# Kernel tuning notes

Hardware: AMD Instinct MI355X
Metric: run time of the kernel (lower is better)

Reference implementation:

```python
import jax, jax.numpy as jnp
import numpy as np

REG = 1.0
LAM1 = REG * 0.1
LAM2 = REG * 0.15
TAU = 0.01
RHO = 1.99
SIGMA = 1.0 / TAU / 72.0


def epsilon(I):
    # I: (c,h,w,2) -> G: (c,h,w,4); symmetrized gradient stencil
    I0, I1 = I[..., 0], I[..., 1]
    g0 = I0 - jnp.pad(I0[:, :-1, :], ((0, 0), (1, 0), (0, 0)))
    g1 = jnp.pad(I0[:, :, 1:] - I0[:, :, :-1], ((0, 0), (0, 0), (1, 0)))
    g2 = I1 - jnp.pad(I1[:, :, :-1], ((0, 0), (0, 0), (1, 0)))
    g3 = jnp.pad(I1[:, 1:, :] - I1[:, :-1, :], ((0, 0), (0, 1), (0, 0)))
    return jnp.stack([g0, g1, g2, g3], axis=-1)


def epsilonT(G):
    # G: (c,h,w,4) -> I: (c,h,w,2); adjoint of epsilon
    g0, g1, g2, g3 = G[..., 0], G[..., 1], G[..., 2], G[..., 3]
    i0 = g0 - jnp.pad(g0[:, 1:, :], ((0, 0), (0, 1), (0, 0)))
    A = g1[:, :, 1:]
    i0 = i0 + jnp.pad(A, ((0, 0), (0, 0), (1, 0))) - jnp.pad(A, ((0, 0), (0, 0), (0, 1)))
    i1 = g2 - jnp.pad(g2[:, :, 1:], ((0, 0), (0, 0), (0, 1)))
    B = g3[:, :-1, :]
    i1 = i1 + jnp.pad(B, ((0, 0), (1, 0), (0, 0))) - jnp.pad(B, ((0, 0), (0, 1), (0, 0)))
    return jnp.stack([i0, i1], axis=-1)


def nabla(I):
    # I: (c,h,w) -> G: (c,h,w,2); forward differences, zero at far boundary
    g0 = jnp.pad(I[:, 1:, :] - I[:, :-1, :], ((0, 0), (0, 1), (0, 0)))
    g1 = jnp.pad(I[:, :, 1:] - I[:, :, :-1], ((0, 0), (0, 0), (0, 1)))
    return jnp.stack([g0, g1], axis=-1)


def nablaT(G):
    # G: (c,h,w,2) -> I: (c,h,w); negative divergence (adjoint of nabla)
    A = G[:, :-1, :, 0]
    B = G[:, :, :-1, 1]
    return (jnp.pad(A, ((0, 0), (1, 0), (0, 0))) - jnp.pad(A, ((0, 0), (0, 1), (0, 0)))
            + jnp.pad(B, ((0, 0), (0, 0), (1, 0))) - jnp.pad(B, ((0, 0), (0, 0), (0, 1))))


def prox_tau_fx(x, y):
    return (x + TAU * y) / (1.0 + TAU)


def prox_tau_fr(r):
    left = jnp.sqrt(jnp.sum(r ** 2, axis=3)) / (TAU * LAM1)
    return r - r / jnp.maximum(left, 1.0)[..., None]


def prox_sigma_g_conj(u):
    return u / jnp.maximum(jnp.sqrt(jnp.sum(u ** 2, axis=3)) / LAM2, 1.0)[..., None]


def setup_inputs() -> dict:
    key = jax.random.key(0)
    y = jax.random.normal(key, (3, 512, 512), dtype=jnp.float32)
    return {"y": y, "n_it_max": 30}


def reference(y, n_it_max):
    c, h, w = y.shape
    x2 = y
    r2 = jnp.zeros((c, h, w, 2), dtype=y.dtype)
    u2 = jnp.zeros((c, h, w, 4), dtype=y.dtype)

    def step(carry, _):
        x2, r2, u2 = carry
        tmp = TAU * epsilonT(u2)
        x = prox_tau_fx(x2 - nablaT(tmp), y)
        r = prox_tau_fr(r2 + tmp)
        u = prox_sigma_g_conj(u2 + SIGMA * epsilon(nabla(2.0 * x - x2) - (2.0 * r - r2)))
        x2 = x2 + RHO * (x - x2)
        r2 = r2 + RHO * (r - r2)
        u2 = u2 + RHO * (u - u2)
        return (x2, r2, u2), None

    (x2, r2, u2), _ = jax.lax.scan(step, (x2, r2, u2), None, length=n_it_max)
    return (x2, r2, u2)
```

## Files before the change

kernel.cpp:

```cpp
#include <hip/hip_runtime.h>
#include <type_traits>


#define H 512
#define W 512
#define C 3
#define HW (H * W)
#define CHW (C * H * W)
#define N_IT 30

#define TW 64
#define TH 16

#define TAU     0.01f
#define LAM2    0.15f
#define RHO     1.99f
#define SIGMA   1.3888888888888888f
#define TL1     0.001f
#define INV_1PT (1.0f / 1.01f)

#define BROWS 18
#define BSTR  72

typedef _Float16 f16;
typedef __attribute__((ext_vector_type(4))) _Float16 h4;
typedef __attribute__((ext_vector_type(8))) _Float16 h8;


template <int MODE>
__global__ __launch_bounds__(384)
void fused_it(const float* __restrict__ y,
              const float* __restrict__ srcX,
              const f16*   __restrict__ srcH,
              float*       __restrict__ dstX,
              f16*         __restrict__ dstH,
              float*       __restrict__ outp)
{
    __shared__ float sb[3][BROWS][BSTR];

    const int tid = threadIdx.x;
    const int c   = blockIdx.z;
    const int i0  = blockIdx.y * TH;
    const int j0  = blockIdx.x * TW;
    const int cb  = c * HW;

    const bool edge = (MODE == 0) ||
                      (blockIdx.x == 0) || (blockIdx.x == W / TW - 1) ||
                      (blockIdx.y == 0) || (blockIdx.y == H / TH - 1);

    const f16* rSrc = srcH;
    const f16* uSrc = srcH + 2 * CHW;
    f16* rDst = dstH;
    f16* uDst = dstH ? dstH + 2 * CHW : nullptr;

    float cu0[4], cu1[4], cu2[4], cu3[4];
    float xbO[4], rb0O[4], rb1O[4];

    auto strip1 = [&](auto SAFE_c, int rr, int s, bool interior) {
        constexpr bool SAFE = decltype(SAFE_c)::value;
        const int gi  = i0 + rr;
        const int gjb = j0 + s;
        const int p   = cb + gi * W + gjb;

        const bool rowC  = SAFE || ((unsigned)gi < H);
        const bool cMain = SAFE || ((unsigned)gjb < W);
        const bool okC   = rowC && cMain;

        float yv[4], x2c[4], r0c[4], r1c[4];
        if (okC) {
            *(float4*)yv = *(const float4*)(y + p);
        } else {
            yv[0] = yv[1] = yv[2] = yv[3] = 0.f;
        }
        if (MODE != 0) {
            if (okC) {
                *(float4*)x2c = *(const float4*)(srcX + p);
                const h8 rv = *(const h8*)(rSrc + 2 * p);
                #pragma unroll
                for (int e = 0; e < 4; ++e) {
                    r0c[e] = (float)rv[2 * e];
                    r1c[e] = (float)rv[2 * e + 1];
                }
            } else {
                #pragma unroll
                for (int e = 0; e < 4; ++e) { x2c[e] = 0.f; r0c[e] = 0.f; r1c[e] = 0.f; }
            }
        }

        float t0c[4], t1c[4], t0n[4], t1w[4];
        if (MODE == 0) {
            #pragma unroll
            for (int e = 0; e < 4; ++e) {
                x2c[e] = yv[e]; r0c[e] = 0.f; r1c[e] = 0.f;
                t0c[e] = t1c[e] = t0n[e] = t1w[e] = 0.f;
            }
            if (interior) {
                #pragma unroll
                for (int e = 0; e < 4; ++e) { cu0[e] = cu1[e] = cu2[e] = cu3[e] = 0.f; }
            }
        } else {
            const bool rowN = SAFE || ((unsigned)(gi - 1) < H);
            const bool rowS = SAFE || ((unsigned)(gi + 1) < H);
            const bool cm1  = SAFE || ((unsigned)(gjb - 1) < W);
            const bool c4   = SAFE || ((unsigned)(gjb + 4) < W);
            const int pN = p - W, pS = p + W;

            auto L4 = [&](int pp, bool ok) -> h4 {
                h4 z = {}; if (ok) z = *(const h4*)(uSrc + 4 * pp); return z;
            };
            auto L8 = [&](int pp, bool ok) -> h8 {
                h8 z = {}; if (ok) z = *(const h8*)(uSrc + 4 * pp); return z;
            };
            const h4 nA = L4(pN - 1, rowN && cm1);
            const h8 nB = L8(pN,     rowN && cMain);
            const h8 nC = L8(pN + 2, rowN && cMain);
            const h4 nD = L4(pN + 4, rowN && c4);
            const h4 cA = L4(p - 1,  rowC && cm1);
            const h8 cB = L8(p,      okC);
            const h8 cC = L8(p + 2,  okC);
            const h4 cD = L4(p + 4,  rowC && c4);
            const h8 sB = L8(pS,     rowS && cMain);
            const h8 sC = L8(pS + 2, rowS && cMain);

            const float u0c[4] = {(float)cB[0], (float)cB[4], (float)cC[0], (float)cC[4]};
            const float u1c[5] = {(float)cB[1], (float)cB[5], (float)cC[1], (float)cC[5], (float)cD[1]};
            const float u2r[6] = {(float)cA[2], (float)cB[2], (float)cB[6], (float)cC[2], (float)cC[6], (float)cD[2]};
            const float u3c[5] = {(float)cA[3], (float)cB[3], (float)cB[7], (float)cC[3], (float)cC[7]};
            const float u0n[4] = {(float)nB[0], (float)nB[4], (float)nC[0], (float)nC[4]};
            const float u1n[5] = {(float)nB[1], (float)nB[5], (float)nC[1], (float)nC[5], (float)nD[1]};
            const float u3n[5] = {(float)nA[3], (float)nB[3], (float)nB[7], (float)nC[3], (float)nC[7]};
            const float u0s[4] = {(float)sB[0], (float)sB[4], (float)sC[0], (float)sC[4]};

            if constexpr (SAFE) {
                #pragma unroll
                for (int e = 0; e < 4; ++e) {
                    t0c[e] = TAU * (u0c[e] - u0s[e] + u1c[e] - u1c[e + 1]);
                    t1c[e] = TAU * (u2r[e + 1] - u2r[e + 2] + u3n[e + 1] - u3c[e + 1]);
                    t0n[e] = TAU * (u0n[e] - u0c[e] + u1n[e] - u1n[e + 1]);
                    t1w[e] = TAU * (u2r[e] - u2r[e + 1] + u3n[e] - u3c[e]);
                }
            } else {
                const bool im0 = gi > 0, imHl = gi < H - 1;
                #pragma unroll
                for (int e = 0; e < 4; ++e) {
                    const int gj = gjb + e;
                    const bool jm0 = gj > 0;
                    t0c[e] = TAU * (u0c[e] - u0s[e] + (jm0 ? u1c[e] : 0.f) - u1c[e + 1]);
                    t1c[e] = TAU * (u2r[e + 1] - u2r[e + 2] + u3n[e + 1] - (imHl ? u3c[e + 1] : 0.f));
                    t0n[e] = im0 ? TAU * (u0n[e] - u0c[e] + (jm0 ? u1n[e] : 0.f) - u1n[e + 1]) : 0.f;
                    t1w[e] = jm0 ? TAU * (u2r[e] - u2r[e + 1] + u3n[e] - (imHl ? u3c[e] : 0.f)) : 0.f;
                }
            }
            if (interior) {
                #pragma unroll
                for (int e = 0; e < 4; ++e) {
                    cu0[e] = u0c[e]; cu1[e] = u1c[e];
                    cu2[e] = u2r[e + 1]; cu3[e] = u3c[e + 1];
                }
            }
        }

        float xnew[4], rn0[4], rn1[4], xb[4], rb0[4], rb1[4];
        {
            const bool imH = SAFE ? true : (gi < H - 1);
            #pragma unroll
            for (int e = 0; e < 4; ++e) {
                const int gj = gjb + e;
                const bool jmW = SAFE ? true : (gj < W - 1);
                const float nT  = t0n[e] - (imH ? t0c[e] : 0.f) + t1w[e] - (jmW ? t1c[e] : 0.f);
                const float xv  = (x2c[e] - nT + TAU * yv[e]) * INV_1PT;
                xb[e] = 2.f * xv - x2c[e];
                const float rp0 = r0c[e] + t0c[e];
                const float rp1 = r1c[e] + t1c[e];
                const float ss  = rp0 * rp0 + rp1 * rp1;
                const float f   = 1.f - fminf(TL1 * rsqrtf(ss), 1.f);
                const float rv0 = rp0 * f, rv1 = rp1 * f;
                rb0[e]  = 2.f * rv0 - r0c[e];
                rb1[e]  = 2.f * rv1 - r1c[e];
                xnew[e] = x2c[e] + RHO * (xv - x2c[e]);
                rn0[e]  = r0c[e] + RHO * (rv0 - r0c[e]);
                rn1[e]  = r1c[e] + RHO * (rv1 - r1c[e]);
            }
        }
        *(float4*)&sb[0][rr + 1][s + 4] = *(float4*)xb;
        *(float4*)&sb[1][rr + 1][s + 4] = *(float4*)rb0;
        *(float4*)&sb[2][rr + 1][s + 4] = *(float4*)rb1;

        if (interior) {
            #pragma unroll
            for (int e = 0; e < 4; ++e) {
                xbO[e] = xb[e]; rb0O[e] = rb0[e]; rb1O[e] = rb1[e];
            }
            if (MODE == 2) {
                *(float4*)(outp + p) = *(float4*)xnew;
                *(float4*)(outp + CHW + 2 * p)     = make_float4(rn0[0], rn1[0], rn0[1], rn1[1]);
                *(float4*)(outp + CHW + 2 * p + 4) = make_float4(rn0[2], rn1[2], rn0[3], rn1[3]);
            } else {
                *(float4*)(dstX + p) = *(float4*)xnew;
                h8 hr;
                #pragma unroll
                for (int e = 0; e < 4; ++e) {
                    hr[2 * e]     = (f16)rn0[e];
                    hr[2 * e + 1] = (f16)rn1[e];
                }
                *(h8*)(rDst + 2 * p) = hr;
            }
        }
    };

    auto ringmap = [&](int t, int& rr, int& s) {
        if (t < 18)      { rr = -1;      s = 4 * t - 4; }
        else if (t < 36) { rr = TH;      s = 4 * (t - 18) - 4; }
        else if (t < 36 + TH) { rr = t - 36;      s = -4; }
        else                  { rr = t - 36 - TH; s = TW; }
    };

    if (!edge) {
        if (tid < 256) {
            strip1(std::true_type{}, tid >> 4, 4 * (tid & 15), true);
        } else if (tid < 256 + 36 + 2 * TH) {
            int rr, s; ringmap(tid - 256, rr, s);
            strip1(std::true_type{}, rr, s, false);
        }
    } else {
        if (tid < 256) {
            strip1(std::false_type{}, tid >> 4, 4 * (tid & 15), true);
        } else if (tid < 256 + 36 + 2 * TH) {
            int rr, s; ringmap(tid - 256, rr, s);
            strip1(std::false_type{}, rr, s, false);
        }
    }
    __syncthreads();

    auto stage2 = [&](auto SAFE_c) {
        constexpr bool SAFE = decltype(SAFE_c)::value;
        const int tx = tid & 15, ty = tid >> 4;
        const int gi  = i0 + ty;
        const int gjb = j0 + 4 * tx;
        const int lr  = ty + 1;
        const int lc  = 4 * tx + 4;
        float4 v;
        float xA[6], xS[6], xN[4], r0C[5], r0N[4], r1C[5], r1S[4];
        xA[0] = sb[0][lr][lc - 1];
        xA[1] = xbO[0]; xA[2] = xbO[1]; xA[3] = xbO[2]; xA[4] = xbO[3];
        xA[5] = sb[0][lr][lc + 4];
        xS[0] = sb[0][lr + 1][lc - 1];
        v = *(const float4*)&sb[0][lr + 1][lc]; xS[1]=v.x; xS[2]=v.y; xS[3]=v.z; xS[4]=v.w;
        xS[5] = sb[0][lr + 1][lc + 4];
        v = *(const float4*)&sb[0][lr - 1][lc]; xN[0]=v.x; xN[1]=v.y; xN[2]=v.z; xN[3]=v.w;
        r0C[0] = sb[1][lr][lc - 1];
        r0C[1] = rb0O[0]; r0C[2] = rb0O[1]; r0C[3] = rb0O[2]; r0C[4] = rb0O[3];
        v = *(const float4*)&sb[1][lr - 1][lc]; r0N[0]=v.x; r0N[1]=v.y; r0N[2]=v.z; r0N[3]=v.w;
        r1C[0] = sb[2][lr][lc - 1];
        r1C[1] = rb1O[0]; r1C[2] = rb1O[1]; r1C[3] = rb1O[2]; r1C[4] = rb1O[3];
        v = *(const float4*)&sb[2][lr + 1][lc]; r1S[0]=v.x; r1S[1]=v.y; r1S[2]=v.z; r1S[3]=v.w;

        const bool im0 = SAFE ? true : (gi > 0);
        const bool imH = SAFE ? true : (gi < H - 1);
        float un0[4], un1[4], un2[4], un3[4];
        #pragma unroll
        for (int e = 0; e < 4; ++e) {
            const int gj = gjb + e;
            const bool jm0 = SAFE ? true : (gj > 0);
            const bool jmW = SAFE ? true : (gj < W - 1);
            const float xC = xA[e + 1], xE = xA[e + 2], xW_ = xA[e];
            const float I0c = (imH ? xS[e + 1] - xC : 0.f) - r0C[e + 1];
            const float I0n = im0 ? (xC - xN[e] - r0N[e]) : 0.f;
            const float I0w = jm0 ? ((imH ? xS[e] - xW_ : 0.f) - r0C[e]) : 0.f;
            const float I1c = (jmW ? xE - xC : 0.f) - r1C[e + 1];
            const float I1w = jm0 ? (xC - xW_ - r1C[e]) : 0.f;
            const float I1s = imH ? ((jmW ? xS[e + 2] - xS[e + 1] : 0.f) - r1S[e]) : 0.f;
            const float g0 = I0c - I0n;
            const float g1 = jm0 ? (I0c - I0w) : 0.f;
            const float g2 = I1c - I1w;
            const float g3 = imH ? (I1s - I1c) : 0.f;
            const float up0 = cu0[e] + SIGMA * g0;
            const float up1 = cu1[e] + SIGMA * g1;
            const float up2 = cu2[e] + SIGMA * g2;
            const float up3 = cu3[e] + SIGMA * g3;
            const float ss  = up0 * up0 + up1 * up1 + up2 * up2 + up3 * up3;
            const float inv = fminf(LAM2 * rsqrtf(ss), 1.f);
            un0[e] = cu0[e] + RHO * (up0 * inv - cu0[e]);
            un1[e] = cu1[e] + RHO * (up1 * inv - cu1[e]);
            un2[e] = cu2[e] + RHO * (up2 * inv - cu2[e]);
            un3[e] = cu3[e] + RHO * (up3 * inv - cu3[e]);
        }
        const int p = cb + gi * W + gjb;
        if (MODE == 2) {
            #pragma unroll
            for (int e = 0; e < 4; ++e)
                *(float4*)(outp + 3 * CHW + 4 * (p + e)) =
                    make_float4(un0[e], un1[e], un2[e], un3[e]);
        } else {
            h8 w0, w1;
            #pragma unroll
            for (int e = 0; e < 2; ++e) {
                w0[4 * e + 0] = (f16)un0[e]; w0[4 * e + 1] = (f16)un1[e];
                w0[4 * e + 2] = (f16)un2[e]; w0[4 * e + 3] = (f16)un3[e];
            }
            #pragma unroll
            for (int e = 2; e < 4; ++e) {
                w1[4 * (e - 2) + 0] = (f16)un0[e]; w1[4 * (e - 2) + 1] = (f16)un1[e];
                w1[4 * (e - 2) + 2] = (f16)un2[e]; w1[4 * (e - 2) + 3] = (f16)un3[e];
            }
            *(h8*)(uDst + 4 * p)     = w0;
            *(h8*)(uDst + 4 * p + 8) = w1;
        }
    };

    if (tid < 256) {
        if (!edge) stage2(std::true_type{});
        else       stage2(std::false_type{});
    }
}

extern "C" void kernel_launch(void* const* d_in, const int* in_sizes, int n_in,
                              void* d_out, int out_size, void* d_ws, size_t ws_size,
                              hipStream_t stream) {
    const float* y = (const float*)d_in[0];
    float* out = (float*)d_out;

    float* x0 = (float*)d_ws;
    float* x1 = x0 + CHW;
    f16*   h0 = (f16*)(x1 + CHW);
    f16*   h1 = h0 + 6 * CHW;

    dim3 blk(384, 1, 1);
    dim3 grd(W / TW, H / TH, C);

    fused_it<0><<<grd, blk, 0, stream>>>(y, nullptr, nullptr, x0, h0, nullptr);
    for (int k = 2; k < N_IT; ++k) {
        const bool even = (k % 2 == 0);
        float* sx = even ? x0 : x1;  f16* sh = even ? h0 : h1;
        float* dx = even ? x1 : x0;  f16* dh = even ? h1 : h0;
        fused_it<1><<<grd, blk, 0, stream>>>(y, sx, sh, dx, dh, nullptr);
    }
    fused_it<2><<<grd, blk, 0, stream>>>(y, x0, h0, nullptr, nullptr, out);
}
```

Measured before the change: 331.5 us.

## Fuse two PDHG iterations per kernel launch using halo tiles in shared memory

Result: faster. 299.7 us (median of 2 runs) (-9.6%).

```diff
diff --git a/kernel.cpp b/kernel.cpp
--- a/kernel.cpp
+++ b/kernel.cpp
@@ -7,7 +7,7 @@
 #define C 3
 #define HW (H * W)
 #define CHW (C * H * W)
-#define N_IT 30
+#define NPAIR 15
 
 #define TW 64
 #define TH 16
@@ -19,8 +19,12 @@
 #define TL1     0.001f
 #define INV_1PT (1.0f / 1.01f)
 
-#define BROWS 18
-#define BSTR  72
+#define AR 22
+#define AC 78
+#define BR 18
+#define BC 72
+#define UR 20
+#define UC 75
 
 typedef _Float16 f16;
 typedef __attribute__((ext_vector_type(4))) _Float16 h4;
@@ -28,15 +32,17 @@
 
 
 template <int MODE>
-__global__ __launch_bounds__(384)
-void fused_it(const float* __restrict__ y,
-              const float* __restrict__ srcX,
-              const f16*   __restrict__ srcH,
-              float*       __restrict__ dstX,
-              f16*         __restrict__ dstH,
-              float*       __restrict__ outp)
+__global__ __launch_bounds__(256)
+void fused2(const float* __restrict__ y,
+            const float* __restrict__ srcX,
+            const f16*   __restrict__ srcH,
+            float*       __restrict__ dstX,
+            f16*         __restrict__ dstH,
+            float*       __restrict__ outp)
 {
-    __shared__ float sb[3][BROWS][BSTR];
+    __shared__ float sbA[3][AR][AC];
+    __shared__ float sbB[3][BR][BC];
+    __shared__ f16   su[UR][UC][4];
 
     const int tid = threadIdx.x;
     const int c   = blockIdx.z;
@@ -53,211 +59,116 @@
     f16* rDst = dstH;
     f16* uDst = dstH ? dstH + 2 * CHW : nullptr;
 
-    float cu0[4], cu1[4], cu2[4], cu3[4];
-    float xbO[4], rb0O[4], rb1O[4];
-
-    auto strip1 = [&](auto SAFE_c, int rr, int s, bool interior) {
-        constexpr bool SAFE = decltype(SAFE_c)::value;
-        const int gi  = i0 + rr;
-        const int gjb = j0 + s;
-        const int p   = cb + gi * W + gjb;
-
+    auto prox1 = [&](auto SAFE_c, int gi, int gjb,
+                     const float* yv, const float* x2c, const float* r0c, const float* r1c,
+                     const float* t0c, const float* t1c, const float* t0n, const float* t1w,
+                     float* xb, float* rb0, float* rb1,
+                     float* xn, float* rn0, float* rn1) {
+        constexpr bool SAFE = decltype(SAFE_c)::value;
+        const bool imH = SAFE ? true : (gi < H - 1);
+        #pragma unroll
+        for (int e = 0; e < 4; ++e) {
+            const int gj = gjb + e;
+            const bool jmW = SAFE ? true : (gj < W - 1);
+            const float nT  = t0n[e] - (imH ? t0c[e] : 0.f) + t1w[e] - (jmW ? t1c[e] : 0.f);
+            const float xv  = (x2c[e] - nT + TAU * yv[e]) * INV_1PT;
+            xb[e] = 2.f * xv - x2c[e];
+            const float rp0 = r0c[e] + t0c[e];
+            const float rp1 = r1c[e] + t1c[e];
+            const float ss  = rp0 * rp0 + rp1 * rp1;
+            const float f   = 1.f - fminf(TL1 * rsqrtf(ss), 1.f);
+            const float rv0 = rp0 * f, rv1 = rp1 * f;
+            rb0[e] = 2.f * rv0 - r0c[e];
+            rb1[e] = 2.f * rv1 - r1c[e];
+            xn[e]  = x2c[e] + RHO * (xv - x2c[e]);
+            rn0[e] = r0c[e] + RHO * (rv0 - r0c[e]);
+            rn1[e] = r1c[e] + RHO * (rv1 - r1c[e]);
+        }
+    };
+
+    auto tGlob = [&](auto SAFE_c, int gi, int gjb, int p,
+                     float* t0c, float* t1c, float* t0n, float* t1w) {
+        constexpr bool SAFE = decltype(SAFE_c)::value;
         const bool rowC  = SAFE || ((unsigned)gi < H);
         const bool cMain = SAFE || ((unsigned)gjb < W);
         const bool okC   = rowC && cMain;
-
-        float yv[4], x2c[4], r0c[4], r1c[4];
-        if (okC) {
-            *(float4*)yv = *(const float4*)(y + p);
+        const bool rowN = SAFE || ((unsigned)(gi - 1) < H);
+        const bool rowS = SAFE || ((unsigned)(gi + 1) < H);
+        const bool cm1  = SAFE || ((unsigned)(gjb - 1) < W);
+        const bool c4   = SAFE || ((unsigned)(gjb + 4) < W);
+        const int pN = p - W, pS = p + W;
+        auto L4 = [&](int pp, bool ok) -> h4 { h4 z = {}; if (ok) z = *(const h4*)(uSrc + 4 * pp); return z; };
+        auto L8 = [&](int pp, bool ok) -> h8 { h8 z = {}; if (ok) z = *(const h8*)(uSrc + 4 * pp); return z; };
+        const h4 nA = L4(pN - 1, rowN && cm1);
+        const h8 nB = L8(pN,     rowN && cMain);
+        const h8 nC = L8(pN + 2, rowN && cMain);
+        const h4 nD = L4(pN + 4, rowN && c4);
+        const h4 cA = L4(p - 1,  rowC && cm1);
+        const h8 cB = L8(p,      okC);
+        const h8 cC = L8(p + 2,  okC);
+        const h4 cD = L4(p + 4,  rowC && c4);
+        const h8 sB = L8(pS,     rowS && cMain);
+        const h8 sC = L8(pS + 2, rowS && cMain);
+
+        const float u0c[4] = {(float)cB[0], (float)cB[4], (float)cC[0], (float)cC[4]};
+        const float u1c[5] = {(float)cB[1], (float)cB[5], (float)cC[1], (float)cC[5], (float)cD[1]};
+        const float u2r[6] = {(float)cA[2], (float)cB[2], (float)cB[6], (float)cC[2], (float)cC[6], (float)cD[2]};
+        const float u3c[5] = {(float)cA[3], (float)cB[3], (float)cB[7], (float)cC[3], (float)cC[7]};
+        const float u0n[4] = {(float)nB[0], (float)nB[4], (float)nC[0], (float)nC[4]};
+        const float u1n[5] = {(float)nB[1], (float)nB[5], (float)nC[1], (float)nC[5], (float)nD[1]};
+        const float u3n[5] = {(float)nA[3], (float)nB[3], (float)nB[7], (float)nC[3], (float)nC[7]};
+        const float u0s[4] = {(float)sB[0], (float)sB[4], (float)sC[0], (float)sC[4]};
+
+        if constexpr (SAFE) {
+            #pragma unroll
+            for (int e = 0; e < 4; ++e) {
+                t0c[e] = TAU * (u0c[e] - u0s[e] + u1c[e] - u1c[e + 1]);
+                t1c[e] = TAU * (u2r[e + 1] - u2r[e + 2] + u3n[e + 1] - u3c[e + 1]);
+                t0n[e] = TAU * (u0n[e] - u0c[e] + u1n[e] - u1n[e + 1]);
+                t1w[e] = TAU * (u2r[e] - u2r[e + 1] + u3n[e] - u3c[e]);
+            }
         } else {
-            yv[0] = yv[1] = yv[2] = yv[3] = 0.f;
-        }
-        if (MODE != 0) {
-            if (okC) {
-                *(float4*)x2c = *(const float4*)(srcX + p);
-                const h8 rv = *(const h8*)(rSrc + 2 * p);
-                #pragma unroll
-                for (int e = 0; e < 4; ++e) {
-                    r0c[e] = (float)rv[2 * e];
-                    r1c[e] = (float)rv[2 * e + 1];
-                }
-            } else {
-                #pragma unroll
-                for (int e = 0; e < 4; ++e) { x2c[e] = 0.f; r0c[e] = 0.f; r1c[e] = 0.f; }
-            }
-        }
-
-        float t0c[4], t1c[4], t0n[4], t1w[4];
-        if (MODE == 0) {
-            #pragma unroll
-            for (int e = 0; e < 4; ++e) {
-                x2c[e] = yv[e]; r0c[e] = 0.f; r1c[e] = 0.f;
-                t0c[e] = t1c[e] = t0n[e] = t1w[e] = 0.f;
-            }
-            if (interior) {
-                #pragma unroll
-                for (int e = 0; e < 4; ++e) { cu0[e] = cu1[e] = cu2[e] = cu3[e] = 0.f; }
-            }
-        } else {
-            const bool rowN = SAFE || ((unsigned)(gi - 1) < H);
-            const bool rowS = SAFE || ((unsigned)(gi + 1) < H);
-            const bool cm1  = SAFE || ((unsigned)(gjb - 1) < W);
-            const bool c4   = SAFE || ((unsigned)(gjb + 4) < W);
-            const int pN = p - W, pS = p + W;
-
-            auto L4 = [&](int pp, bool ok) -> h4 {
-                h4 z = {}; if (ok) z = *(const h4*)(uSrc + 4 * pp); return z;
-            };
-            auto L8 = [&](int pp, bool ok) -> h8 {
-                h8 z = {}; if (ok) z = *(const h8*)(uSrc + 4 * pp); return z;
-            };
-            const h4 nA = L4(pN - 1, rowN && cm1);
-            const h8 nB = L8(pN,     rowN && cMain);
-            const h8 nC = L8(pN + 2, rowN && cMain);
-            const h4 nD = L4(pN + 4, rowN && c4);
-            const h4 cA = L4(p - 1,  rowC && cm1);
-            const h8 cB = L8(p,      okC);
-            const h8 cC = L8(p + 2,  okC);
-            const h4 cD = L4(p + 4,  rowC && c4);
-            const h8 sB = L8(pS,     rowS && cMain);
-            const h8 sC = L8(pS + 2, rowS && cMain);
-
-            const float u0c[4] = {(float)cB[0], (float)cB[4], (float)cC[0], (float)cC[4]};
-            const float u1c[5] = {(float)cB[1], (float)cB[5], (float)cC[1], (float)cC[5], (float)cD[1]};
-            const float u2r[6] = {(float)cA[2], (float)cB[2], (float)cB[6], (float)cC[2], (float)cC[6], (float)cD[2]};
-            const float u3c[5] = {(float)cA[3], (float)cB[3], (float)cB[7], (float)cC[3], (float)cC[7]};
-            const float u0n[4] = {(float)nB[0], (float)nB[4], (float)nC[0], (float)nC[4]};
-            const float u1n[5] = {(float)nB[1], (float)nB[5], (float)nC[1], (float)nC[5], (float)nD[1]};
-            const float u3n[5] = {(float)nA[3], (float)nB[3], (float)nB[7], (float)nC[3], (float)nC[7]};
-            const float u0s[4] = {(float)sB[0], (float)sB[4], (float)sC[0], (float)sC[4]};
-
-            if constexpr (SAFE) {
-                #pragma unroll
-                for (int e = 0; e < 4; ++e) {
-                    t0c[e] = TAU * (u0c[e] - u0s[e] + u1c[e] - u1c[e + 1]);
-                    t1c[e] = TAU * (u2r[e + 1] - u2r[e + 2] + u3n[e + 1] - u3c[e + 1]);
-                    t0n[e] = TAU * (u0n[e] - u0c[e] + u1n[e] - u1n[e + 1]);
-                    t1w[e] = TAU * (u2r[e] - u2r[e + 1] + u3n[e] - u3c[e]);
-                }
-            } else {
-                const bool im0 = gi > 0, imHl = gi < H - 1;
-                #pragma unroll
-                for (int e = 0; e < 4; ++e) {
-                    const int gj = gjb + e;
-                    const bool jm0 = gj > 0;
-                    t0c[e] = TAU * (u0c[e] - u0s[e] + (jm0 ? u1c[e] : 0.f) - u1c[e + 1]);
-                    t1c[e] = TAU * (u2r[e + 1] - u2r[e + 2] + u3n[e + 1] - (imHl ? u3c[e + 1] : 0.f));
-                    t0n[e] = im0 ? TAU * (u0n[e] - u0c[e] + (jm0 ? u1n[e] : 0.f) - u1n[e + 1]) : 0.f;
-                    t1w[e] = jm0 ? TAU * (u2r[e] - u2r[e + 1] + u3n[e] - (imHl ? u3c[e] : 0.f)) : 0.f;
-                }
-            }
-            if (interior) {
-                #pragma unroll
-                for (int e = 0; e < 4; ++e) {
-                    cu0[e] = u0c[e]; cu1[e] = u1c[e];
-                    cu2[e] = u2r[e + 1]; cu3[e] = u3c[e + 1];
-                }
-            }
-        }
-
-        float xnew[4], rn0[4], rn1[4], xb[4], rb0[4], rb1[4];
-        {
-            const bool imH = SAFE ? true : (gi < H - 1);
+            const bool im0 = gi > 0, imHl = gi < H - 1;
             #pragma unroll
             for (int e = 0; e < 4; ++e) {
                 const int gj = gjb + e;
-                const bool jmW = SAFE ? true : (gj < W - 1);
-                const float nT  = t0n[e] - (imH ? t0c[e] : 0.f) + t1w[e] - (jmW ? t1c[e] : 0.f);
-                const float xv  = (x2c[e] - nT + TAU * yv[e]) * INV_1PT;
-                xb[e] = 2.f * xv - x2c[e];
-                const float rp0 = r0c[e] + t0c[e];
-                const float rp1 = r1c[e] + t1c[e];
-                const float ss  = rp0 * rp0 + rp1 * rp1;
-                const float f   = 1.f - fminf(TL1 * rsqrtf(ss), 1.f);
-                const float rv0 = rp0 * f, rv1 = rp1 * f;
-                rb0[e]  = 2.f * rv0 - r0c[e];
-                rb1[e]  = 2.f * rv1 - r1c[e];
-                xnew[e] = x2c[e] + RHO * (xv - x2c[e]);
-                rn0[e]  = r0c[e] + RHO * (rv0 - r0c[e]);
-                rn1[e]  = r1c[e] + RHO * (rv1 - r1c[e]);
-            }
-        }
-        *(float4*)&sb[0][rr + 1][s + 4] = *(float4*)xb;
-        *(float4*)&sb[1][rr + 1][s + 4] = *(float4*)rb0;
-        *(float4*)&sb[2][rr + 1][s + 4] = *(float4*)rb1;
-
-        if (interior) {
-            #pragma unroll
-            for (int e = 0; e < 4; ++e) {
-                xbO[e] = xb[e]; rb0O[e] = rb0[e]; rb1O[e] = rb1[e];
-            }
-            if (MODE == 2) {
-                *(float4*)(outp + p) = *(float4*)xnew;
-                *(float4*)(outp + CHW + 2 * p)     = make_float4(rn0[0], rn1[0], rn0[1], rn1[1]);
-                *(float4*)(outp + CHW + 2 * p + 4) = make_float4(rn0[2], rn1[2], rn0[3], rn1[3]);
-            } else {
-                *(float4*)(dstX + p) = *(float4*)xnew;
-                h8 hr;
-                #pragma unroll
-                for (int e = 0; e < 4; ++e) {
-                    hr[2 * e]     = (f16)rn0[e];
-                    hr[2 * e + 1] = (f16)rn1[e];
-                }
-                *(h8*)(rDst + 2 * p) = hr;
-            }
-        }
-    };
-
-    auto ringmap = [&](int t, int& rr, int& s) {
-        if (t < 18)      { rr = -1;      s = 4 * t - 4; }
-        else if (t < 36) { rr = TH;      s = 4 * (t - 18) - 4; }
-        else if (t < 36 + TH) { rr = t - 36;      s = -4; }
-        else                  { rr = t - 36 - TH; s = TW; }
-    };
-
-    if (!edge) {
-        if (tid < 256) {
-            strip1(std::true_type{}, tid >> 4, 4 * (tid & 15), true);
-        } else if (tid < 256 + 36 + 2 * TH) {
-            int rr, s; ringmap(tid - 256, rr, s);
-            strip1(std::true_type{}, rr, s, false);
-        }
-    } else {
-        if (tid < 256) {
-            strip1(std::false_type{}, tid >> 4, 4 * (tid & 15), true);
-        } else if (tid < 256 + 36 + 2 * TH) {
-            int rr, s; ringmap(tid - 256, rr, s);
-            strip1(std::false_type{}, rr, s, false);
-        }
-    }
-    __syncthreads();
-
-    auto stage2 = [&](auto SAFE_c) {
-        constexpr bool SAFE = decltype(SAFE_c)::value;
-        const int tx = tid & 15, ty = tid >> 4;
-        const int gi  = i0 + ty;
-        const int gjb = j0 + 4 * tx;
-        const int lr  = ty + 1;
-        const int lc  = 4 * tx + 4;
+                const bool jm0 = gj > 0;
+                t0c[e] = TAU * (u0c[e] - u0s[e] + (jm0 ? u1c[e] : 0.f) - u1c[e + 1]);
+                t1c[e] = TAU * (u2r[e + 1] - u2r[e + 2] + u3n[e + 1] - (imHl ? u3c[e + 1] : 0.f));
+                t0n[e] = im0 ? TAU * (u0n[e] - u0c[e] + (jm0 ? u1n[e] : 0.f) - u1n[e + 1]) : 0.f;
+                t1w[e] = jm0 ? TAU * (u2r[e] - u2r[e + 1] + u3n[e] - (imHl ? u3c[e] : 0.f)) : 0.f;
+            }
+        }
+    };
+
+    auto loadA = [&](int rr, int s,
+                     float* xA, float* xS, float* xN,
+                     float* r0C, float* r0N, float* r1C, float* r1S) {
+        const int lr = rr + 3, lc = s + 8;
         float4 v;
-        float xA[6], xS[6], xN[4], r0C[5], r0N[4], r1C[5], r1S[4];
-        xA[0] = sb[0][lr][lc - 1];
-        xA[1] = xbO[0]; xA[2] = xbO[1]; xA[3] = xbO[2]; xA[4] = xbO[3];
-        xA[5] = sb[0][lr][lc + 4];
-        xS[0] = sb[0][lr + 1][lc - 1];
-        v = *(const float4*)&sb[0][lr + 1][lc]; xS[1]=v.x; xS[2]=v.y; xS[3]=v.z; xS[4]=v.w;
-        xS[5] = sb[0][lr + 1][lc + 4];
-        v = *(const float4*)&sb[0][lr - 1][lc]; xN[0]=v.x; xN[1]=v.y; xN[2]=v.z; xN[3]=v.w;
-        r0C[0] = sb[1][lr][lc - 1];
-        r0C[1] = rb0O[0]; r0C[2] = rb0O[1]; r0C[3] = rb0O[2]; r0C[4] = rb0O[3];
-        v = *(const float4*)&sb[1][lr - 1][lc]; r0N[0]=v.x; r0N[1]=v.y; r0N[2]=v.z; r0N[3]=v.w;
-        r1C[0] = sb[2][lr][lc - 1];
-        r1C[1] = rb1O[0]; r1C[2] = rb1O[1]; r1C[3] = rb1O[2]; r1C[4] = rb1O[3];
-        v = *(const float4*)&sb[2][lr + 1][lc]; r1S[0]=v.x; r1S[1]=v.y; r1S[2]=v.z; r1S[3]=v.w;
-
+        xA[0] = sbA[0][lr][lc - 1];
+        v = *(const float4*)&sbA[0][lr][lc]; xA[1]=v.x; xA[2]=v.y; xA[3]=v.z; xA[4]=v.w;
+        xA[5] = sbA[0][lr][lc + 4];
+        xS[0] = sbA[0][lr + 1][lc - 1];
+        v = *(const float4*)&sbA[0][lr + 1][lc]; xS[1]=v.x; xS[2]=v.y; xS[3]=v.z; xS[4]=v.w;
+        xS[5] = sbA[0][lr + 1][lc + 4];
+        v = *(const float4*)&sbA[0][lr - 1][lc]; xN[0]=v.x; xN[1]=v.y; xN[2]=v.z; xN[3]=v.w;
+        r0C[0] = sbA[1][lr][lc - 1];
+        v = *(const float4*)&sbA[1][lr][lc]; r0C[1]=v.x; r0C[2]=v.y; r0C[3]=v.z; r0C[4]=v.w;
+        v = *(const float4*)&sbA[1][lr - 1][lc]; r0N[0]=v.x; r0N[1]=v.y; r0N[2]=v.z; r0N[3]=v.w;
+        r1C[0] = sbA[2][lr][lc - 1];
+        v = *(const float4*)&sbA[2][lr][lc]; r1C[1]=v.x; r1C[2]=v.y; r1C[3]=v.z; r1C[4]=v.w;
+        v = *(const float4*)&sbA[2][lr + 1][lc]; r1S[0]=v.x; r1S[1]=v.y; r1S[2]=v.z; r1S[3]=v.w;
+    };
+
+    auto s2core = [&](auto SAFE_c, int gi, int gjb,
+                      const float* xA, const float* xS, const float* xN,
+                      const float* r0C, const float* r0N, const float* r1C, const float* r1S,
+                      const float* cu0, const float* cu1, const float* cu2, const float* cu3,
+                      float* un0, float* un1, float* un2, float* un3) {
+        constexpr bool SAFE = decltype(SAFE_c)::value;
         const bool im0 = SAFE ? true : (gi > 0);
         const bool imH = SAFE ? true : (gi < H - 1);
-        float un0[4], un1[4], un2[4], un3[4];
         #pragma unroll
         for (int e = 0; e < 4; ++e) {
             const int gj = gjb + e;
@@ -285,7 +196,243 @@
             un2[e] = cu2[e] + RHO * (up2 * inv - cu2[e]);
             un3[e] = cu3[e] + RHO * (up3 * inv - cu3[e]);
         }
-        const int p = cb + gi * W + gjb;
+    };
+
+    auto phaseA = [&](auto SAFE_c) {
+        constexpr bool SAFE = decltype(SAFE_c)::value;
+        for (int idx = tid; idx < AR * 18; idx += 256) {
+            const int rw = idx / 18, rr = rw - 3;
+            const int s  = 4 * (idx - rw * 18) - 4;
+            const int gi = i0 + rr, gjb = j0 + s;
+            const int p  = cb + gi * W + gjb;
+            const bool rowC  = SAFE || ((unsigned)gi < H);
+            const bool cMain = SAFE || ((unsigned)gjb < W);
+            const bool okC   = rowC && cMain;
+
+            float yv[4], x2c[4], r0c[4], r1c[4];
+            if (okC) { *(float4*)yv = *(const float4*)(y + p); }
+            else     { yv[0] = yv[1] = yv[2] = yv[3] = 0.f; }
+
+            float t0c[4], t1c[4], t0n[4], t1w[4];
+            if (MODE == 0) {
+                #pragma unroll
+                for (int e = 0; e < 4; ++e) {
+                    x2c[e] = yv[e]; r0c[e] = 0.f; r1c[e] = 0.f;
+                    t0c[e] = t1c[e] = t0n[e] = t1w[e] = 0.f;
+                }
+            } else {
+                if (okC) {
+                    *(float4*)x2c = *(const float4*)(srcX + p);
+                    const h8 rv = *(const h8*)(rSrc + 2 * p);
+                    #pragma unroll
+                    for (int e = 0; e < 4; ++e) {
+                        r0c[e] = (float)rv[2 * e];
+                        r1c[e] = (float)rv[2 * e + 1];
+                    }
+                } else {
+                    #pragma unroll
+                    for (int e = 0; e < 4; ++e) { x2c[e] = 0.f; r0c[e] = 0.f; r1c[e] = 0.f; }
+                }
+                tGlob(SAFE_c, gi, gjb, p, t0c, t1c, t0n, t1w);
+            }
+
+            float xb[4], rb0[4], rb1[4], xn[4], rn0[4], rn1[4];
+            prox1(SAFE_c, gi, gjb, yv, x2c, r0c, r1c, t0c, t1c, t0n, t1w,
+                  xb, rb0, rb1, xn, rn0, rn1);
+
+            *(float4*)&sbA[0][rr + 3][s + 8] = *(float4*)xb;
+            *(float4*)&sbA[1][rr + 3][s + 8] = *(float4*)rb0;
+            *(float4*)&sbA[2][rr + 3][s + 8] = *(float4*)rb1;
+            if (rr >= -1 && rr <= 16) {
+                *(float4*)&sbB[0][rr + 1][s + 4] = *(float4*)xn;
+                *(float4*)&sbB[1][rr + 1][s + 4] = *(float4*)rn0;
+                *(float4*)&sbB[2][rr + 1][s + 4] = *(float4*)rn1;
+            }
+        }
+    };
+
+    auto phaseB = [&](auto SAFE_c) {
+        constexpr bool SAFE = decltype(SAFE_c)::value;
+        for (int idx = tid; idx < UR * 18; idx += 256) {
+            const int rw = idx / 18, rr = rw - 2;
+            const int s  = 4 * (idx - rw * 18) - 4;
+            const int gi = i0 + rr, gjb = j0 + s;
+            const int p  = cb + gi * W + gjb;
+
+            float xA[6], xS[6], xN[4], r0C[5], r0N[4], r1C[5], r1S[4];
+            loadA(rr, s, xA, xS, xN, r0C, r0N, r1C, r1S);
+
+            float cu0[4], cu1[4], cu2[4], cu3[4];
+            if (MODE == 0) {
+                #pragma unroll
+                for (int e = 0; e < 4; ++e) { cu0[e] = cu1[e] = cu2[e] = cu3[e] = 0.f; }
+            } else {
+                const bool okC = SAFE || (((unsigned)gi < H) && ((unsigned)gjb < W));
+                if (okC) {
+                    const h8 a = *(const h8*)(uSrc + 4 * p);
+                    const h8 b = *(const h8*)(uSrc + 4 * p + 8);
+                    cu0[0]=(float)a[0]; cu1[0]=(float)a[1]; cu2[0]=(float)a[2]; cu3[0]=(float)a[3];
+                    cu0[1]=(float)a[4]; cu1[1]=(float)a[5]; cu2[1]=(float)a[6]; cu3[1]=(float)a[7];
+                    cu0[2]=(float)b[0]; cu1[2]=(float)b[1]; cu2[2]=(float)b[2]; cu3[2]=(float)b[3];
+                    cu0[3]=(float)b[4]; cu1[3]=(float)b[5]; cu2[3]=(float)b[6]; cu3[3]=(float)b[7];
+                } else {
+                    #pragma unroll
+                    for (int e = 0; e < 4; ++e) { cu0[e] = cu1[e] = cu2[e] = cu3[e] = 0.f; }
+                }
+            }
+
+            float un0[4], un1[4], un2[4], un3[4];
+            s2core(SAFE_c, gi, gjb, xA, xS, xN, r0C, r0N, r1C, r1S,
+                   cu0, cu1, cu2, cu3, un0, un1, un2, un3);
+
+            const int ur = rr + 2, uc = s + 6;
+            if constexpr (SAFE) {
+                h8 w0, w1;
+                #pragma unroll
+                for (int e = 0; e < 2; ++e) {
+                    w0[4*e+0]=(f16)un0[e]; w0[4*e+1]=(f16)un1[e];
+                    w0[4*e+2]=(f16)un2[e]; w0[4*e+3]=(f16)un3[e];
+                }
+                #pragma unroll
+                for (int e = 2; e < 4; ++e) {
+                    w1[4*(e-2)+0]=(f16)un0[e]; w1[4*(e-2)+1]=(f16)un1[e];
+                    w1[4*(e-2)+2]=(f16)un2[e]; w1[4*(e-2)+3]=(f16)un3[e];
+                }
+                *(h8*)&su[ur][uc][0]     = w0;
+                *(h8*)&su[ur][uc + 2][0] = w1;
+            } else {
+                #pragma unroll
+                for (int e = 0; e < 4; ++e) {
+                    const int gj = gjb + e;
+                    const bool ok = ((unsigned)gi < H) && ((unsigned)gj < W);
+                    h4 hv = {};
+                    if (ok) { hv[0]=(f16)un0[e]; hv[1]=(f16)un1[e]; hv[2]=(f16)un2[e]; hv[3]=(f16)un3[e]; }
+                    *(h4*)&su[ur][uc + e][0] = hv;
+                }
+            }
+        }
+    };
+
+    auto phaseC = [&](auto SAFE_c) {
+        constexpr bool SAFE = decltype(SAFE_c)::value;
+        for (int idx = tid; idx < BR * 18; idx += 256) {
+            const int rw = idx / 18, rr = rw - 1;
+            const int s  = 4 * (idx - rw * 18) - 4;
+            const int gi = i0 + rr, gjb = j0 + s;
+            const int p  = cb + gi * W + gjb;
+            const bool okC = SAFE || (((unsigned)gi < H) && ((unsigned)gjb < W));
+
+            float yv[4];
+            if (okC) { *(float4*)yv = *(const float4*)(y + p); }
+            else     { yv[0] = yv[1] = yv[2] = yv[3] = 0.f; }
+
+            float x2c[4], r0c[4], r1c[4];
+            *(float4*)x2c = *(const float4*)&sbB[0][rr + 1][s + 4];
+            *(float4*)r0c = *(const float4*)&sbB[1][rr + 1][s + 4];
+            *(float4*)r1c = *(const float4*)&sbB[2][rr + 1][s + 4];
+
+            h4 pN_[6], pC_[6], pS_[4];
+            #pragma unroll
+            for (int k = 0; k < 6; ++k) {
+                pN_[k] = *(const h4*)&su[rr + 1][s + 5 + k][0];
+                pC_[k] = *(const h4*)&su[rr + 2][s + 5 + k][0];
+            }
+            #pragma unroll
+            for (int k = 0; k < 4; ++k)
+                pS_[k] = *(const h4*)&su[rr + 3][s + 6 + k][0];
+
+            const float u0c[4] = {(float)pC_[1][0], (float)pC_[2][0], (float)pC_[3][0], (float)pC_[4][0]};
+            const float u1c[5] = {(float)pC_[1][1], (float)pC_[2][1], (float)pC_[3][1], (float)pC_[4][1], (float)pC_[5][1]};
+            const float u2r[6] = {(float)pC_[0][2], (float)pC_[1][2], (float)pC_[2][2], (float)pC_[3][2], (float)pC_[4][2], (float)pC_[5][2]};
+            const float u3c[5] = {(float)pC_[0][3], (float)pC_[1][3], (float)pC_[2][3], (float)pC_[3][3], (float)pC_[4][3]};
+            const float u0n[4] = {(float)pN_[1][0], (float)pN_[2][0], (float)pN_[3][0], (float)pN_[4][0]};
+            const float u1n[5] = {(float)pN_[1][1], (float)pN_[2][1], (float)pN_[3][1], (float)pN_[4][1], (float)pN_[5][1]};
+            const float u3n[5] = {(float)pN_[0][3], (float)pN_[1][3], (float)pN_[2][3], (float)pN_[3][3], (float)pN_[4][3]};
+            const float u0s[4] = {(float)pS_[0][0], (float)pS_[1][0], (float)pS_[2][0], (float)pS_[3][0]};
+
+            float t0c[4], t1c[4], t0n[4], t1w[4];
+            if constexpr (SAFE) {
+                #pragma unroll
+                for (int e = 0; e < 4; ++e) {
+                    t0c[e] = TAU * (u0c[e] - u0s[e] + u1c[e] - u1c[e + 1]);
+                    t1c[e] = TAU * (u2r[e + 1] - u2r[e + 2] + u3n[e + 1] - u3c[e + 1]);
+                    t0n[e] = TAU * (u0n[e] - u0c[e] + u1n[e] - u1n[e + 1]);
+                    t1w[e] = TAU * (u2r[e] - u2r[e + 1] + u3n[e] - u3c[e]);
+                }
+            } else {
+                const bool im0 = gi > 0, imHl = gi < H - 1;
+                #pragma unroll
+                for (int e = 0; e < 4; ++e) {
+                    const int gj = gjb + e;
+                    const bool jm0 = gj > 0;
+                    t0c[e] = TAU * (u0c[e] - u0s[e] + (jm0 ? u1c[e] : 0.f) - u1c[e + 1]);
+                    t1c[e] = TAU * (u2r[e + 1] - u2r[e + 2] + u3n[e + 1] - (imHl ? u3c[e + 1] : 0.f));
+                    t0n[e] = im0 ? TAU * (u0n[e] - u0c[e] + (jm0 ? u1n[e] : 0.f) - u1n[e + 1]) : 0.f;
+                    t1w[e] = jm0 ? TAU * (u2r[e] - u2r[e + 1] + u3n[e] - (imHl ? u3c[e] : 0.f)) : 0.f;
+                }
+            }
+
+            float xb[4], rb0[4], rb1[4], xn[4], rn0[4], rn1[4];
+            prox1(SAFE_c, gi, gjb, yv, x2c, r0c, r1c, t0c, t1c, t0n, t1w,
+                  xb, rb0, rb1, xn, rn0, rn1);
+
+            *(float4*)&sbA[0][rr + 3][s + 8] = *(float4*)xb;
+            *(float4*)&sbA[1][rr + 3][s + 8] = *(float4*)rb0;
+            *(float4*)&sbA[2][rr + 3][s + 8] = *(float4*)rb1;
+
+            if ((unsigned)rr < 16 && (unsigned)s < 64) {
+                if (MODE == 2) {
+                    *(float4*)(outp + p) = *(float4*)xn;
+                    *(float4*)(outp + CHW + 2 * p)     = make_float4(rn0[0], rn1[0], rn0[1], rn1[1]);
+                    *(float4*)(outp + CHW + 2 * p + 4) = make_float4(rn0[2], rn1[2], rn0[3], rn1[3]);
+                } else {
+                    *(float4*)(dstX + p) = *(float4*)xn;
+                    h8 hr;
+                    #pragma unroll
+                    for (int e = 0; e < 4; ++e) {
+                        hr[2 * e]     = (f16)rn0[e];
+                        hr[2 * e + 1] = (f16)rn1[e];
+                    }
+                    *(h8*)(rDst + 2 * p) = hr;
+                }
+            }
+        }
+    };
+
+    if (!edge) phaseA(std::true_type{});  else phaseA(std::false_type{});
+    __syncthreads();
+    if (!edge) phaseB(std::true_type{});  else phaseB(std::false_type{});
+    __syncthreads();
+    if (!edge) phaseC(std::true_type{});  else phaseC(std::false_type{});
+    __syncthreads();
+
+    {
+        const int rr = tid >> 4;
+        const int s  = 4 * (tid & 15);
+        const int gi = i0 + rr, gjb = j0 + s;
+        const int p  = cb + gi * W + gjb;
+
+        float xA[6], xS[6], xN[4], r0C[5], r0N[4], r1C[5], r1S[4];
+        loadA(rr, s, xA, xS, xN, r0C, r0N, r1C, r1S);
+
+        float cu0[4], cu1[4], cu2[4], cu3[4];
+        {
+            const h8 a = *(const h8*)&su[rr + 2][s + 6][0];
+            const h8 b = *(const h8*)&su[rr + 2][s + 8][0];
+            cu0[0]=(float)a[0]; cu1[0]=(float)a[1]; cu2[0]=(float)a[2]; cu3[0]=(float)a[3];
+            cu0[1]=(float)a[4]; cu1[1]=(float)a[5]; cu2[1]=(float)a[6]; cu3[1]=(float)a[7];
+            cu0[2]=(float)b[0]; cu1[2]=(float)b[1]; cu2[2]=(float)b[2]; cu3[2]=(float)b[3];
+            cu0[3]=(float)b[4]; cu1[3]=(float)b[5]; cu2[3]=(float)b[6]; cu3[3]=(float)b[7];
+        }
+
+        float un0[4], un1[4], un2[4], un3[4];
+        if (!edge)
+            s2core(std::true_type{},  gi, gjb, xA, xS, xN, r0C, r0N, r1C, r1S,
+                   cu0, cu1, cu2, cu3, un0, un1, un2, un3);
+        else
+            s2core(std::false_type{}, gi, gjb, xA, xS, xN, r0C, r0N, r1C, r1S,
+                   cu0, cu1, cu2, cu3, un0, un1, un2, un3);
+
         if (MODE == 2) {
             #pragma unroll
             for (int e = 0; e < 4; ++e)
@@ -295,22 +442,17 @@
             h8 w0, w1;
             #pragma unroll
             for (int e = 0; e < 2; ++e) {
-                w0[4 * e + 0] = (f16)un0[e]; w0[4 * e + 1] = (f16)un1[e];
-                w0[4 * e + 2] = (f16)un2[e]; w0[4 * e + 3] = (f16)un3[e];
+                w0[4*e+0]=(f16)un0[e]; w0[4*e+1]=(f16)un1[e];
+                w0[4*e+2]=(f16)un2[e]; w0[4*e+3]=(f16)un3[e];
             }
             #pragma unroll
             for (int e = 2; e < 4; ++e) {
-                w1[4 * (e - 2) + 0] = (f16)un0[e]; w1[4 * (e - 2) + 1] = (f16)un1[e];
-                w1[4 * (e - 2) + 2] = (f16)un2[e]; w1[4 * (e - 2) + 3] = (f16)un3[e];
+                w1[4*(e-2)+0]=(f16)un0[e]; w1[4*(e-2)+1]=(f16)un1[e];
+                w1[4*(e-2)+2]=(f16)un2[e]; w1[4*(e-2)+3]=(f16)un3[e];
             }
             *(h8*)(uDst + 4 * p)     = w0;
             *(h8*)(uDst + 4 * p + 8) = w1;
         }
-    };
-
-    if (tid < 256) {
-        if (!edge) stage2(std::true_type{});
-        else       stage2(std::false_type{});
     }
 }
 
@@ -325,15 +467,15 @@
     f16*   h0 = (f16*)(x1 + CHW);
     f16*   h1 = h0 + 6 * CHW;
 
-    dim3 blk(384, 1, 1);
+    dim3 blk(256, 1, 1);
     dim3 grd(W / TW, H / TH, C);
 
-    fused_it<0><<<grd, blk, 0, stream>>>(y, nullptr, nullptr, x0, h0, nullptr);
-    for (int k = 2; k < N_IT; ++k) {
-        const bool even = (k % 2 == 0);
-        float* sx = even ? x0 : x1;  f16* sh = even ? h0 : h1;
-        float* dx = even ? x1 : x0;  f16* dh = even ? h1 : h0;
-        fused_it<1><<<grd, blk, 0, stream>>>(y, sx, sh, dx, dh, nullptr);
+    fused2<0><<<grd, blk, 0, stream>>>(y, nullptr, nullptr, x0, h0, nullptr);
+    for (int i = 1; i < NPAIR - 1; ++i) {
+        const bool even = (i % 2 == 0);
+        float* sx = even ? x1 : x0;  f16* sh = even ? h1 : h0;
+        float* dx = even ? x0 : x1;  f16* dh = even ? h0 : h1;
+        fused2<1><<<grd, blk, 0, stream>>>(y, sx, sh, dx, dh, nullptr);
     }
-    fused_it<2><<<grd, blk, 0, stream>>>(y, x0, h0, nullptr, nullptr, out);
+    fused2<2><<<grd, blk, 0, stream>>>(y, x1, h1, nullptr, nullptr, out);
 }
```
